# Kernel tuning notes

Hardware: AMD Instinct MI355X
Metric: run time of the kernel (lower is better)

Reference implementation:

```python
import jax, jax.numpy as jnp
import numpy as np

ALIGN_CORNERS = True
APPLY_SMOOTHSTEP = True

SIZES = [(32, 32, 32), (64, 64, 64), (128, 128, 128), (256, 256, 256)]
FEAT_DIMS = [4, 4, 4, 4]
N_POINTS = 1048576  # 2**20 sample points (e.g. 8192 rays x 128 samples)


def setup_inputs() -> dict:
    key = jax.random.key(0)
    ks = jax.random.split(key, 1 + len(SIZES))
    # grid_sample-style coords in [-1, 1], layout [1, 1, 1, N, 3] (x, y, z)
    grid = jax.random.uniform(ks[0], (1, 1, 1, N_POINTS, 3), dtype=jnp.float32) * 2.0 - 1.0
    inp = {"grid": grid}
    for i, (size, c) in enumerate(zip(SIZES, FEAT_DIMS)):
        # original init: (rand(1,C,1,1,1)*2-1).repeat over spatial; use randn volumes for a
        # non-degenerate baseline (same shapes/math path)
        inp[f"vol{i}"] = jax.random.normal(ks[1 + i], (1, c, *size), dtype=jnp.float32)
    return inp


def _smooth_sample(vol, grid_pts):
    """Trilinear sample with border padding, align_corners=True, smoothstep weights.

    vol: [C, D, H, W]; grid_pts: [P, 3] with (x, y, z) in [-1, 1].
    Returns [C, P].
    """
    C, D, H, W = vol.shape
    # unnormalize (align_corners=True): [-1,1] -> [0, dim-1]; border padding via clip
    x = jnp.clip((grid_pts[:, 0] + 1.0) * 0.5 * (W - 1), 0.0, W - 1)
    y = jnp.clip((grid_pts[:, 1] + 1.0) * 0.5 * (H - 1), 0.0, H - 1)
    z = jnp.clip((grid_pts[:, 2] + 1.0) * 0.5 * (D - 1), 0.0, D - 1)

    x0 = jnp.floor(x); y0 = jnp.floor(y); z0 = jnp.floor(z)
    tx = x - x0; ty = y - y0; tz = z - z0
    if APPLY_SMOOTHSTEP:
        tx = tx * tx * (3.0 - 2.0 * tx)
        ty = ty * ty * (3.0 - 2.0 * ty)
        tz = tz * tz * (3.0 - 2.0 * tz)

    x0i = x0.astype(jnp.int32); x1i = jnp.minimum(x0i + 1, W - 1)
    y0i = y0.astype(jnp.int32); y1i = jnp.minimum(y0i + 1, H - 1)
    z0i = z0.astype(jnp.int32); z1i = jnp.minimum(z0i + 1, D - 1)

    # 8 corner gathers -> [C, P]
    c000 = vol[:, z0i, y0i, x0i]; c001 = vol[:, z0i, y0i, x1i]
    c010 = vol[:, z0i, y1i, x0i]; c011 = vol[:, z0i, y1i, x1i]
    c100 = vol[:, z1i, y0i, x0i]; c101 = vol[:, z1i, y0i, x1i]
    c110 = vol[:, z1i, y1i, x0i]; c111 = vol[:, z1i, y1i, x1i]

    c00 = c000 + (c001 - c000) * tx
    c01 = c010 + (c011 - c010) * tx
    c10 = c100 + (c101 - c100) * tx
    c11 = c110 + (c111 - c110) * tx
    c0 = c00 + (c01 - c00) * ty
    c1 = c10 + (c11 - c10) * ty
    return c0 + (c1 - c0) * tz


def reference(grid, vol0, vol1, vol2, vol3):
    # grid: [1, 1, 1, N, 3] -> [N, 3]
    pts = grid.reshape(-1, 3)
    n = pts.shape[0]
    out = []
    for vol in (vol0, vol1, vol2, vol3):
        feat = _smooth_sample(vol[0], pts)            # [C, N]
        out.append(feat.reshape(1, -1, 1, 1, n))      # grid_sample output layout
    return jnp.concatenate(out, axis=1)               # [1, sum(C), 1, 1, N]
```

## Files before the change

### kernel.cpp

```cpp
#include <hip/hip_runtime.h>

#define NPTS 1048576
#define NB 32
#define NBINS (NB * NB * NB)

typedef float v4f __attribute__((ext_vector_type(4)));

__device__ __forceinline__ void nt_store4(const float4& f, float4* p) {
    __builtin_nontemporal_store(*(const v4f*)&f, (v4f*)p);
}


__device__ __forceinline__ float4 lerp4(const float4 a, const float4 b, const float t) {
    return make_float4(a.x + (b.x - a.x) * t,
                       a.y + (b.y - a.y) * t,
                       a.z + (b.z - a.z) * t,
                       a.w + (b.w - a.w) * t);
}

struct CoordW { float tx, ty, tz; int b00, b01, b10, b11, x0, x1; };

template<int D>
__device__ __forceinline__ CoordW mkcoord(float gx, float gy, float gz) {
    CoordW c;
    float x = fminf(fmaxf((gx + 1.0f) * (0.5f * (float)(D - 1)), 0.0f), (float)(D - 1));
    float y = fminf(fmaxf((gy + 1.0f) * (0.5f * (float)(D - 1)), 0.0f), (float)(D - 1));
    float z = fminf(fmaxf((gz + 1.0f) * (0.5f * (float)(D - 1)), 0.0f), (float)(D - 1));
    float xf = floorf(x), yf = floorf(y), zf = floorf(z);
    float tx = x - xf, ty = y - yf, tz = z - zf;
    c.tx = tx * tx * (3.0f - 2.0f * tx);
    c.ty = ty * ty * (3.0f - 2.0f * ty);
    c.tz = tz * tz * (3.0f - 2.0f * tz);
    int x0 = (int)xf, y0 = (int)yf, z0 = (int)zf;
    int y1 = min(y0 + 1, D - 1), z1 = min(z0 + 1, D - 1);
    c.x0 = x0;
    c.x1 = min(x0 + 1, D - 1);
    c.b00 = (z0 * D + y0) * D;
    c.b01 = (z0 * D + y1) * D;
    c.b10 = (z1 * D + y0) * D;
    c.b11 = (z1 * D + y1) * D;
    return c;
}

__device__ __forceinline__ float4 reduce8(const float4* q, const CoordW& c) {
    float4 c00 = lerp4(q[0], q[1], c.tx);
    float4 c01 = lerp4(q[2], q[3], c.tx);
    float4 c10 = lerp4(q[4], q[5], c.tx);
    float4 c11 = lerp4(q[6], q[7], c.tx);
    float4 c0 = lerp4(c00, c01, c.ty);
    float4 c1 = lerp4(c10, c11, c.ty);
    return lerp4(c0, c1, c.tz);
}


#define DHW0 (32 * 32 * 32)
#define DHW1 (64 * 64 * 64)
#define DHW2 (128 * 128 * 128)

__global__ __launch_bounds__(256) void xpose_all_kernel(
    const float* __restrict__ v0, const float* __restrict__ v1, const float* __restrict__ v2,
    float4* __restrict__ w0, float4* __restrict__ w1, float4* __restrict__ w2)
{
    constexpr int B2 = DHW2 / 256, B1 = DHW1 / 256;
    int b = blockIdx.x;
    int t = threadIdx.x;
    if (b < B2) {
        int v = b * 256 + t;
        w2[v] = make_float4(v2[v], v2[v + DHW2], v2[v + 2 * DHW2], v2[v + 3 * DHW2]);
    } else if (b < B2 + B1) {
        int v = (b - B2) * 256 + t;
        w1[v] = make_float4(v1[v], v1[v + DHW1], v1[v + 2 * DHW1], v1[v + 3 * DHW1]);
    } else {
        int v = (b - B2 - B1) * 256 + t;
        w0[v] = make_float4(v0[v], v0[v + DHW0], v0[v + 2 * DHW0], v0[v + 3 * DHW0]);
    }
}


__device__ __forceinline__ int bin_of(float gx, float gy, float gz) {
    float ux = fminf(fmaxf((gx + 1.0f) * 0.5f, 0.0f), 1.0f);
    float uy = fminf(fmaxf((gy + 1.0f) * 0.5f, 0.0f), 1.0f);
    float uz = fminf(fmaxf((gz + 1.0f) * 0.5f, 0.0f), 1.0f);
    int bx = min((int)(ux * (float)NB), NB - 1);
    int by = min((int)(uy * (float)NB), NB - 1);
    int bz = min((int)(uz * (float)NB), NB - 1);
    return (bz * NB + by) * NB + bx;
}

__global__ __launch_bounds__(256) void bin_hist_kernel(const float* __restrict__ grid,
                                                       unsigned* __restrict__ hist) {
    int p = blockIdx.x * blockDim.x + threadIdx.x;
    float gx = grid[3 * p + 0];
    float gy = grid[3 * p + 1];
    float gz = grid[3 * p + 2];
    atomicAdd(&hist[bin_of(gx, gy, gz)], 1u);
}

__global__ __launch_bounds__(1024) void scan_kernel(const unsigned* __restrict__ hist,
                                                    unsigned* __restrict__ offsets) {
    __shared__ unsigned partial[1024];
    const int t = threadIdx.x;
    const int base = t * 32;
    unsigned sum = 0;
#pragma unroll
    for (int i = 0; i < 32; ++i) sum += hist[base + i];
    partial[t] = sum;
    __syncthreads();
    for (int off = 1; off < 1024; off <<= 1) {
        unsigned v = (t >= off) ? partial[t - off] : 0u;
        __syncthreads();
        partial[t] += v;
        __syncthreads();
    }
    unsigned run = partial[t] - sum;
#pragma unroll
    for (int i = 0; i < 32; ++i) {
        offsets[base + i] = run;
        run += hist[base + i];
    }
}

__global__ __launch_bounds__(256) void scatter_kernel(const float* __restrict__ grid,
                                                      unsigned* __restrict__ offsets,
                                                      float4* __restrict__ sorted,
                                                      int* __restrict__ inv) {
    int p = blockIdx.x * blockDim.x + threadIdx.x;
    float gx = grid[3 * p + 0];
    float gy = grid[3 * p + 1];
    float gz = grid[3 * p + 2];
    int b = bin_of(gx, gy, gz);
    unsigned pos = atomicAdd(&offsets[b], 1u);
    sorted[pos] = make_float4(gx, gy, gz, __int_as_float(p));
    inv[p] = (int)pos;
}


__global__ __launch_bounds__(256, 4) void gather_sorted_kernel(
    const float4* __restrict__ sorted,
    const float4* __restrict__ w0, const float4* __restrict__ w1,
    const float4* __restrict__ w2, const float* __restrict__ v3,
    float4* __restrict__ wsout)
{
    int bid = blockIdx.x;
    int sb = (bid & 7) * (int)(gridDim.x >> 3) + (bid >> 3);
    int s = sb * 256 + (int)threadIdx.x;
    float4 gp = sorted[s];
    float gx = gp.x, gy = gp.y, gz = gp.z;

    CoordW c0 = mkcoord<32>(gx, gy, gz);
    CoordW c1 = mkcoord<64>(gx, gy, gz);
    CoordW c2 = mkcoord<128>(gx, gy, gz);
    CoordW c3 = mkcoord<256>(gx, gy, gz);

    float4 qa[8], qb[8], qc[8];
    qa[0] = w0[c0.b00 + c0.x0]; qa[1] = w0[c0.b00 + c0.x1];
    qa[2] = w0[c0.b01 + c0.x0]; qa[3] = w0[c0.b01 + c0.x1];
    qa[4] = w0[c0.b10 + c0.x0]; qa[5] = w0[c0.b10 + c0.x1];
    qa[6] = w0[c0.b11 + c0.x0]; qa[7] = w0[c0.b11 + c0.x1];

    qb[0] = w1[c1.b00 + c1.x0]; qb[1] = w1[c1.b00 + c1.x1];
    qb[2] = w1[c1.b01 + c1.x0]; qb[3] = w1[c1.b01 + c1.x1];
    qb[4] = w1[c1.b10 + c1.x0]; qb[5] = w1[c1.b10 + c1.x1];
    qb[6] = w1[c1.b11 + c1.x0]; qb[7] = w1[c1.b11 + c1.x1];

    qc[0] = w2[c2.b00 + c2.x0]; qc[1] = w2[c2.b00 + c2.x1];
    qc[2] = w2[c2.b01 + c2.x0]; qc[3] = w2[c2.b01 + c2.x1];
    qc[4] = w2[c2.b10 + c2.x0]; qc[5] = w2[c2.b10 + c2.x1];
    qc[6] = w2[c2.b11 + c2.x0]; qc[7] = w2[c2.b11 + c2.x1];

    const int xm = min(c3.x0, 254);
    const bool edge = (c3.x0 == 255);
    float2 qd[16];
#pragma unroll
    for (int ch = 0; ch < 4; ++ch) {
        const float* __restrict__ vc = v3 + (size_t)ch * (256 * 256 * 256);
        qd[ch * 4 + 0] = *(const float2*)(vc + c3.b00 + xm);
        qd[ch * 4 + 1] = *(const float2*)(vc + c3.b01 + xm);
        qd[ch * 4 + 2] = *(const float2*)(vc + c3.b10 + xm);
        qd[ch * 4 + 3] = *(const float2*)(vc + c3.b11 + xm);
    }

    float4 f0 = reduce8(qa, c0);
    float4 f1 = reduce8(qb, c1);
    float4 f2 = reduce8(qc, c2);

    float r3[4];
#pragma unroll
    for (int ch = 0; ch < 4; ++ch) {
        float v00a = edge ? qd[ch * 4 + 0].y : qd[ch * 4 + 0].x, v00b = qd[ch * 4 + 0].y;
        float v01a = edge ? qd[ch * 4 + 1].y : qd[ch * 4 + 1].x, v01b = qd[ch * 4 + 1].y;
        float v10a = edge ? qd[ch * 4 + 2].y : qd[ch * 4 + 2].x, v10b = qd[ch * 4 + 2].y;
        float v11a = edge ? qd[ch * 4 + 3].y : qd[ch * 4 + 3].x, v11b = qd[ch * 4 + 3].y;
        float c00 = v00a + (v00b - v00a) * c3.tx;
        float c01 = v01a + (v01b - v01a) * c3.tx;
        float c10 = v10a + (v10b - v10a) * c3.tx;
        float c11 = v11a + (v11b - v11a) * c3.tx;
        float e0 = c00 + (c01 - c00) * c3.ty;
        float e1 = c10 + (c11 - c10) * c3.ty;
        r3[ch] = e0 + (e1 - e0) * c3.tz;
    }
    float4 f3 = make_float4(r3[0], r3[1], r3[2], r3[3]);

    float4* w = wsout + (size_t)s * 4;
    nt_store4(f0, w + 0);
    nt_store4(f1, w + 1);
    nt_store4(f2, w + 2);
    nt_store4(f3, w + 3);
}


__device__ __forceinline__ void permute_one(const float4* __restrict__ wsout,
                                            const int* __restrict__ inv,
                                            float* __restrict__ out, int p) {
    int s = inv[p];
    const float4* w = wsout + (size_t)s * 4;
    float4 f0 = w[0], f1 = w[1], f2 = w[2], f3 = w[3];
    __builtin_nontemporal_store(f0.x, &out[ 0 * NPTS + p]);
    __builtin_nontemporal_store(f0.y, &out[ 1 * NPTS + p]);
    __builtin_nontemporal_store(f0.z, &out[ 2 * NPTS + p]);
    __builtin_nontemporal_store(f0.w, &out[ 3 * NPTS + p]);
    __builtin_nontemporal_store(f1.x, &out[ 4 * NPTS + p]);
    __builtin_nontemporal_store(f1.y, &out[ 5 * NPTS + p]);
    __builtin_nontemporal_store(f1.z, &out[ 6 * NPTS + p]);
    __builtin_nontemporal_store(f1.w, &out[ 7 * NPTS + p]);
    __builtin_nontemporal_store(f2.x, &out[ 8 * NPTS + p]);
    __builtin_nontemporal_store(f2.y, &out[ 9 * NPTS + p]);
    __builtin_nontemporal_store(f2.z, &out[10 * NPTS + p]);
    __builtin_nontemporal_store(f2.w, &out[11 * NPTS + p]);
    __builtin_nontemporal_store(f3.x, &out[12 * NPTS + p]);
    __builtin_nontemporal_store(f3.y, &out[13 * NPTS + p]);
    __builtin_nontemporal_store(f3.z, &out[14 * NPTS + p]);
    __builtin_nontemporal_store(f3.w, &out[15 * NPTS + p]);
}

__global__ __launch_bounds__(256) void permute_kernel(const float4* __restrict__ wsout,
                                                      const int* __restrict__ inv,
                                                      float* __restrict__ out) {
    int p = blockIdx.x * blockDim.x + threadIdx.x;
    permute_one(wsout, inv, out, p);
    permute_one(wsout, inv, out, p + NPTS / 2);
}


template<int D>
__device__ __forceinline__ float4 sample_inter(const float4* __restrict__ v,
                                               float gx, float gy, float gz) {
    CoordW c = mkcoord<D>(gx, gy, gz);
    float4 q[8];
    q[0] = v[c.b00 + c.x0]; q[1] = v[c.b00 + c.x1];
    q[2] = v[c.b01 + c.x0]; q[3] = v[c.b01 + c.x1];
    q[4] = v[c.b10 + c.x0]; q[5] = v[c.b10 + c.x1];
    q[6] = v[c.b11 + c.x0]; q[7] = v[c.b11 + c.x1];
    return reduce8(q, c);
}

template<int D>
__device__ __forceinline__ float4 sample_direct(const float* __restrict__ v,
                                                float gx, float gy, float gz) {
    CoordW c = mkcoord<D>(gx, gy, gz);
    float r[4];
#pragma unroll
    for (int ch = 0; ch < 4; ++ch) {
        const float* __restrict__ vc = v + (size_t)ch * (D * D * D);
        float c000 = vc[c.b00 + c.x0], c001 = vc[c.b00 + c.x1];
        float c010 = vc[c.b01 + c.x0], c011 = vc[c.b01 + c.x1];
        float c100 = vc[c.b10 + c.x0], c101 = vc[c.b10 + c.x1];
        float c110 = vc[c.b11 + c.x0], c111 = vc[c.b11 + c.x1];
        float c00 = c000 + (c001 - c000) * c.tx;
        float c01 = c010 + (c011 - c010) * c.tx;
        float c10 = c100 + (c101 - c100) * c.tx;
        float c11 = c110 + (c111 - c110) * c.tx;
        float e0 = c00 + (c01 - c00) * c.ty;
        float e1 = c10 + (c11 - c10) * c.ty;
        r[ch] = e0 + (e1 - e0) * c.tz;
    }
    return make_float4(r[0], r[1], r[2], r[3]);
}

__global__ __launch_bounds__(256) void mg_direct_kernel(
    const float* __restrict__ grid,
    const float* __restrict__ v0, const float* __restrict__ v1,
    const float* __restrict__ v2, const float* __restrict__ v3,
    float* __restrict__ out)
{
    int p = blockIdx.x * blockDim.x + threadIdx.x;
    float gx = grid[3 * p + 0];
    float gy = grid[3 * p + 1];
    float gz = grid[3 * p + 2];
    float4 f0 = sample_direct<32>(v0, gx, gy, gz);
    float4 f1 = sample_direct<64>(v1, gx, gy, gz);
    float4 f2 = sample_direct<128>(v2, gx, gy, gz);
    float4 f3 = sample_direct<256>(v3, gx, gy, gz);
    out[ 0 * NPTS + p] = f0.x; out[ 1 * NPTS + p] = f0.y;
    out[ 2 * NPTS + p] = f0.z; out[ 3 * NPTS + p] = f0.w;
    out[ 4 * NPTS + p] = f1.x; out[ 5 * NPTS + p] = f1.y;
    out[ 6 * NPTS + p] = f1.z; out[ 7 * NPTS + p] = f1.w;
    out[ 8 * NPTS + p] = f2.x; out[ 9 * NPTS + p] = f2.y;
    out[10 * NPTS + p] = f2.z; out[11 * NPTS + p] = f2.w;
    out[12 * NPTS + p] = f3.x; out[13 * NPTS + p] = f3.y;
    out[14 * NPTS + p] = f3.z; out[15 * NPTS + p] = f3.w;
}

__global__ __launch_bounds__(256) void mg_inter_kernel(
    const float* __restrict__ grid,
    const float4* __restrict__ w0, const float4* __restrict__ w1,
    const float4* __restrict__ w2, const float* __restrict__ v3,
    float* __restrict__ out)
{
    int p = blockIdx.x * blockDim.x + threadIdx.x;
    float gx = grid[3 * p + 0];
    float gy = grid[3 * p + 1];
    float gz = grid[3 * p + 2];
    float4 f0 = sample_inter<32>(w0, gx, gy, gz);
    float4 f1 = sample_inter<64>(w1, gx, gy, gz);
    float4 f2 = sample_inter<128>(w2, gx, gy, gz);
    float4 f3 = sample_direct<256>(v3, gx, gy, gz);
    out[ 0 * NPTS + p] = f0.x; out[ 1 * NPTS + p] = f0.y;
    out[ 2 * NPTS + p] = f0.z; out[ 3 * NPTS + p] = f0.w;
    out[ 4 * NPTS + p] = f1.x; out[ 5 * NPTS + p] = f1.y;
    out[ 6 * NPTS + p] = f1.z; out[ 7 * NPTS + p] = f1.w;
    out[ 8 * NPTS + p] = f2.x; out[ 9 * NPTS + p] = f2.y;
    out[10 * NPTS + p] = f2.z; out[11 * NPTS + p] = f2.w;
    out[12 * NPTS + p] = f3.x; out[13 * NPTS + p] = f3.y;
    out[14 * NPTS + p] = f3.z; out[15 * NPTS + p] = f3.w;
}


extern "C" void kernel_launch(void* const* d_in, const int* in_sizes, int n_in,
                              void* d_out, int out_size, void* d_ws, size_t ws_size,
                              hipStream_t stream) {
    const float* grid = (const float*)d_in[0];
    const float* v0   = (const float*)d_in[1];
    const float* v1   = (const float*)d_in[2];
    const float* v2   = (const float*)d_in[3];
    const float* v3   = (const float*)d_in[4];
    float* out = (float*)d_out;

    constexpr size_t OFF_WSOUT  = 0;
    constexpr size_t OFF_SORTED = OFF_WSOUT  + (size_t)NPTS * 64;
    constexpr size_t OFF_W2     = OFF_SORTED + (size_t)NPTS * 16;
    constexpr size_t OFF_W1     = OFF_W2     + (size_t)DHW2 * 16;
    constexpr size_t OFF_W0     = OFF_W1     + (size_t)DHW1 * 16;
    constexpr size_t OFF_INV    = OFF_W0     + (size_t)DHW0 * 16;
    constexpr size_t OFF_HIST   = OFF_INV    + (size_t)NPTS * 4;
    constexpr size_t OFF_OFFS   = OFF_HIST   + (size_t)NBINS * 4;
    constexpr size_t WS_FULL    = OFF_OFFS   + (size_t)NBINS * 4;
    constexpr size_t WS_INTER   = (size_t)(DHW0 + DHW1 + DHW2) * 16;

    const int threads = 256;
    const int pt_blocks = NPTS / threads;
    char* ws = (char*)d_ws;

    if (ws_size >= WS_FULL) {
        float4*   wsout  = (float4*)(ws + OFF_WSOUT);
        float4*   sorted = (float4*)(ws + OFF_SORTED);
        float4*   w2     = (float4*)(ws + OFF_W2);
        float4*   w1     = (float4*)(ws + OFF_W1);
        float4*   w0     = (float4*)(ws + OFF_W0);
        int*      inv    = (int*)   (ws + OFF_INV);
        unsigned* hist   = (unsigned*)(ws + OFF_HIST);
        unsigned* offs   = (unsigned*)(ws + OFF_OFFS);

        (void)hipMemsetAsync(hist, 0, (size_t)NBINS * 4, stream);
        xpose_all_kernel<<<(DHW0 + DHW1 + DHW2) / threads, threads, 0, stream>>>(
            v0, v1, v2, w0, w1, w2);
        bin_hist_kernel<<<pt_blocks, threads, 0, stream>>>(grid, hist);
        scan_kernel<<<1, 1024, 0, stream>>>(hist, offs);
        scatter_kernel<<<pt_blocks, threads, 0, stream>>>(grid, offs, sorted, inv);
        gather_sorted_kernel<<<pt_blocks, threads, 0, stream>>>(sorted, w0, w1, w2, v3, wsout);
        permute_kernel<<<pt_blocks / 2, threads, 0, stream>>>(wsout, inv, out);
    } else if (ws_size >= WS_INTER) {
        float4* w0 = (float4*)d_ws;
        float4* w1 = w0 + DHW0;
        float4* w2 = w1 + DHW1;
        xpose_all_kernel<<<(DHW0 + DHW1 + DHW2) / threads, threads, 0, stream>>>(
            v0, v1, v2, w0, w1, w2);
        mg_inter_kernel<<<pt_blocks, threads, 0, stream>>>(grid, w0, w1, w2, v3, out);
    } else {
        mg_direct_kernel<<<pt_blocks, threads, 0, stream>>>(grid, v0, v1, v2, v3, out);
    }
}
```

Baseline: 662.8 us.

## Fuse transpose with histogram, process two points per thread in gather and permute

Merges the volume-transpose and bin-histogram kernels into one launch, removing a kernel boundary. The sorted gather kernel now handles two points per thread, issuing all corner loads for both before any reduction (enforced with a sched_barrier) to raise memory-level parallelism, with launch bounds relaxed from 4 to 3 waves. The permute kernel handles four points per thread with all loads issued before the stores, and gather results now use regular stores instead of nontemporal ones. The cost is higher register pressure and fewer resident waves per CU.

```diff
diff --git a/kernel.cpp b/kernel.cpp
--- a/kernel.cpp
+++ b/kernel.cpp
@@ -4,11 +4,11 @@
 #define NB 32
 #define NBINS (NB * NB * NB)
 
+#define DHW0 (32 * 32 * 32)
+#define DHW1 (64 * 64 * 64)
+#define DHW2 (128 * 128 * 128)
+
 typedef float v4f __attribute__((ext_vector_type(4)));
-
-__device__ __forceinline__ void nt_store4(const float4& f, float4* p) {
-    __builtin_nontemporal_store(*(const v4f*)&f, (v4f*)p);
-}
 
 
 __device__ __forceinline__ float4 lerp4(const float4 a, const float4 b, const float t) {
@@ -52,16 +52,43 @@
     return lerp4(c0, c1, c.tz);
 }
 
-
-#define DHW0 (32 * 32 * 32)
-#define DHW1 (64 * 64 * 64)
-#define DHW2 (128 * 128 * 128)
-
-__global__ __launch_bounds__(256) void xpose_all_kernel(
+__device__ __forceinline__ float4 reduce_v3(const float2* qd, const CoordW& c, bool edge) {
+    float r[4];
+#pragma unroll
+    for (int ch = 0; ch < 4; ++ch) {
+        float v00a = edge ? qd[ch * 4 + 0].y : qd[ch * 4 + 0].x, v00b = qd[ch * 4 + 0].y;
+        float v01a = edge ? qd[ch * 4 + 1].y : qd[ch * 4 + 1].x, v01b = qd[ch * 4 + 1].y;
+        float v10a = edge ? qd[ch * 4 + 2].y : qd[ch * 4 + 2].x, v10b = qd[ch * 4 + 2].y;
+        float v11a = edge ? qd[ch * 4 + 3].y : qd[ch * 4 + 3].x, v11b = qd[ch * 4 + 3].y;
+        float c00 = v00a + (v00b - v00a) * c.tx;
+        float c01 = v01a + (v01b - v01a) * c.tx;
+        float c10 = v10a + (v10b - v10a) * c.tx;
+        float c11 = v11a + (v11b - v11a) * c.tx;
+        float e0 = c00 + (c01 - c00) * c.ty;
+        float e1 = c10 + (c11 - c10) * c.ty;
+        r[ch] = e0 + (e1 - e0) * c.tz;
+    }
+    return make_float4(r[0], r[1], r[2], r[3]);
+}
+
+
+__device__ __forceinline__ int bin_of(float gx, float gy, float gz) {
+    float ux = fminf(fmaxf((gx + 1.0f) * 0.5f, 0.0f), 1.0f);
+    float uy = fminf(fmaxf((gy + 1.0f) * 0.5f, 0.0f), 1.0f);
+    float uz = fminf(fmaxf((gz + 1.0f) * 0.5f, 0.0f), 1.0f);
+    int bx = min((int)(ux * (float)NB), NB - 1);
+    int by = min((int)(uy * (float)NB), NB - 1);
+    int bz = min((int)(uz * (float)NB), NB - 1);
+    return (bz * NB + by) * NB + bx;
+}
+
+
+__global__ __launch_bounds__(256) void xpose_hist_kernel(
     const float* __restrict__ v0, const float* __restrict__ v1, const float* __restrict__ v2,
-    float4* __restrict__ w0, float4* __restrict__ w1, float4* __restrict__ w2)
+    float4* __restrict__ w0, float4* __restrict__ w1, float4* __restrict__ w2,
+    const float* __restrict__ grid, unsigned* __restrict__ hist)
 {
-    constexpr int B2 = DHW2 / 256, B1 = DHW1 / 256;
+    constexpr int B2 = DHW2 / 256, B1 = DHW1 / 256, B0 = DHW0 / 256;
     int b = blockIdx.x;
     int t = threadIdx.x;
     if (b < B2) {
@@ -70,30 +97,16 @@
     } else if (b < B2 + B1) {
         int v = (b - B2) * 256 + t;
         w1[v] = make_float4(v1[v], v1[v + DHW1], v1[v + 2 * DHW1], v1[v + 3 * DHW1]);
-    } else {
+    } else if (b < B2 + B1 + B0) {
         int v = (b - B2 - B1) * 256 + t;
         w0[v] = make_float4(v0[v], v0[v + DHW0], v0[v + 2 * DHW0], v0[v + 3 * DHW0]);
-    }
-}
-
-
-__device__ __forceinline__ int bin_of(float gx, float gy, float gz) {
-    float ux = fminf(fmaxf((gx + 1.0f) * 0.5f, 0.0f), 1.0f);
-    float uy = fminf(fmaxf((gy + 1.0f) * 0.5f, 0.0f), 1.0f);
-    float uz = fminf(fmaxf((gz + 1.0f) * 0.5f, 0.0f), 1.0f);
-    int bx = min((int)(ux * (float)NB), NB - 1);
-    int by = min((int)(uy * (float)NB), NB - 1);
-    int bz = min((int)(uz * (float)NB), NB - 1);
-    return (bz * NB + by) * NB + bx;
-}
-
-__global__ __launch_bounds__(256) void bin_hist_kernel(const float* __restrict__ grid,
-                                                       unsigned* __restrict__ hist) {
-    int p = blockIdx.x * blockDim.x + threadIdx.x;
-    float gx = grid[3 * p + 0];
-    float gy = grid[3 * p + 1];
-    float gz = grid[3 * p + 2];
-    atomicAdd(&hist[bin_of(gx, gy, gz)], 1u);
+    } else {
+        int p = (b - B2 - B1 - B0) * 256 + t;
+        float gx = grid[3 * p + 0];
+        float gy = grid[3 * p + 1];
+        float gz = grid[3 * p + 2];
+        atomicAdd(&hist[bin_of(gx, gy, gz)], 1u);
+    }
 }
 
 __global__ __launch_bounds__(1024) void scan_kernel(const unsigned* __restrict__ hist,
@@ -135,7 +148,7 @@
 }
 
 
-__global__ __launch_bounds__(256, 4) void gather_sorted_kernel(
+__global__ __launch_bounds__(256, 3) void gather_sorted_kernel(
     const float4* __restrict__ sorted,
     const float4* __restrict__ w0, const float4* __restrict__ w1,
     const float4* __restrict__ w2, const float* __restrict__ v3,
@@ -143,78 +156,96 @@
 {
     int bid = blockIdx.x;
     int sb = (bid & 7) * (int)(gridDim.x >> 3) + (bid >> 3);
-    int s = sb * 256 + (int)threadIdx.x;
-    float4 gp = sorted[s];
-    float gx = gp.x, gy = gp.y, gz = gp.z;
-
-    CoordW c0 = mkcoord<32>(gx, gy, gz);
-    CoordW c1 = mkcoord<64>(gx, gy, gz);
-    CoordW c2 = mkcoord<128>(gx, gy, gz);
-    CoordW c3 = mkcoord<256>(gx, gy, gz);
-
-    float4 qa[8], qb[8], qc[8];
-    qa[0] = w0[c0.b00 + c0.x0]; qa[1] = w0[c0.b00 + c0.x1];
-    qa[2] = w0[c0.b01 + c0.x0]; qa[3] = w0[c0.b01 + c0.x1];
-    qa[4] = w0[c0.b10 + c0.x0]; qa[5] = w0[c0.b10 + c0.x1];
-    qa[6] = w0[c0.b11 + c0.x0]; qa[7] = w0[c0.b11 + c0.x1];
-
-    qb[0] = w1[c1.b00 + c1.x0]; qb[1] = w1[c1.b00 + c1.x1];
-    qb[2] = w1[c1.b01 + c1.x0]; qb[3] = w1[c1.b01 + c1.x1];
-    qb[4] = w1[c1.b10 + c1.x0]; qb[5] = w1[c1.b10 + c1.x1];
-    qb[6] = w1[c1.b11 + c1.x0]; qb[7] = w1[c1.b11 + c1.x1];
-
-    qc[0] = w2[c2.b00 + c2.x0]; qc[1] = w2[c2.b00 + c2.x1];
-    qc[2] = w2[c2.b01 + c2.x0]; qc[3] = w2[c2.b01 + c2.x1];
-    qc[4] = w2[c2.b10 + c2.x0]; qc[5] = w2[c2.b10 + c2.x1];
-    qc[6] = w2[c2.b11 + c2.x0]; qc[7] = w2[c2.b11 + c2.x1];
-
-    const int xm = min(c3.x0, 254);
-    const bool edge = (c3.x0 == 255);
-    float2 qd[16];
+    int base = sb * 512 + (int)threadIdx.x;
+    int sA = base, sB = base + 256;
+    float4 gpA = sorted[sA];
+    float4 gpB = sorted[sB];
+
+    CoordW c0A = mkcoord<32>(gpA.x, gpA.y, gpA.z);
+    CoordW c1A = mkcoord<64>(gpA.x, gpA.y, gpA.z);
+    CoordW c2A = mkcoord<128>(gpA.x, gpA.y, gpA.z);
+    CoordW c3A = mkcoord<256>(gpA.x, gpA.y, gpA.z);
+    CoordW c0B = mkcoord<32>(gpB.x, gpB.y, gpB.z);
+    CoordW c1B = mkcoord<64>(gpB.x, gpB.y, gpB.z);
+    CoordW c2B = mkcoord<128>(gpB.x, gpB.y, gpB.z);
+    CoordW c3B = mkcoord<256>(gpB.x, gpB.y, gpB.z);
+    const int  xmA = min(c3A.x0, 254);
+    const bool edgeA = (c3A.x0 == 255);
+    const int  xmB = min(c3B.x0, 254);
+    const bool edgeB = (c3B.x0 == 255);
+
+    float4 qaA[8], qbA[8], qcA[8];
+    float2 qdA[16];
+    float4 qaB[8], qbB[8], qcB[8];
+    float2 qdB[16];
+
+    qaA[0] = w0[c0A.b00 + c0A.x0]; qaA[1] = w0[c0A.b00 + c0A.x1];
+    qaA[2] = w0[c0A.b01 + c0A.x0]; qaA[3] = w0[c0A.b01 + c0A.x1];
+    qaA[4] = w0[c0A.b10 + c0A.x0]; qaA[5] = w0[c0A.b10 + c0A.x1];
+    qaA[6] = w0[c0A.b11 + c0A.x0]; qaA[7] = w0[c0A.b11 + c0A.x1];
+
+    qbA[0] = w1[c1A.b00 + c1A.x0]; qbA[1] = w1[c1A.b00 + c1A.x1];
+    qbA[2] = w1[c1A.b01 + c1A.x0]; qbA[3] = w1[c1A.b01 + c1A.x1];
+    qbA[4] = w1[c1A.b10 + c1A.x0]; qbA[5] = w1[c1A.b10 + c1A.x1];
+    qbA[6] = w1[c1A.b11 + c1A.x0]; qbA[7] = w1[c1A.b11 + c1A.x1];
+
+    qcA[0] = w2[c2A.b00 + c2A.x0]; qcA[1] = w2[c2A.b00 + c2A.x1];
+    qcA[2] = w2[c2A.b01 + c2A.x0]; qcA[3] = w2[c2A.b01 + c2A.x1];
+    qcA[4] = w2[c2A.b10 + c2A.x0]; qcA[5] = w2[c2A.b10 + c2A.x1];
+    qcA[6] = w2[c2A.b11 + c2A.x0]; qcA[7] = w2[c2A.b11 + c2A.x1];
+
 #pragma unroll
     for (int ch = 0; ch < 4; ++ch) {
         const float* __restrict__ vc = v3 + (size_t)ch * (256 * 256 * 256);
-        qd[ch * 4 + 0] = *(const float2*)(vc + c3.b00 + xm);
-        qd[ch * 4 + 1] = *(const float2*)(vc + c3.b01 + xm);
-        qd[ch * 4 + 2] = *(const float2*)(vc + c3.b10 + xm);
-        qd[ch * 4 + 3] = *(const float2*)(vc + c3.b11 + xm);
-    }
-
-    float4 f0 = reduce8(qa, c0);
-    float4 f1 = reduce8(qb, c1);
-    float4 f2 = reduce8(qc, c2);
-
-    float r3[4];
+        qdA[ch * 4 + 0] = *(const float2*)(vc + c3A.b00 + xmA);
+        qdA[ch * 4 + 1] = *(const float2*)(vc + c3A.b01 + xmA);
+        qdA[ch * 4 + 2] = *(const float2*)(vc + c3A.b10 + xmA);
+        qdA[ch * 4 + 3] = *(const float2*)(vc + c3A.b11 + xmA);
+    }
+
+    qaB[0] = w0[c0B.b00 + c0B.x0]; qaB[1] = w0[c0B.b00 + c0B.x1];
+    qaB[2] = w0[c0B.b01 + c0B.x0]; qaB[3] = w0[c0B.b01 + c0B.x1];
+    qaB[4] = w0[c0B.b10 + c0B.x0]; qaB[5] = w0[c0B.b10 + c0B.x1];
+    qaB[6] = w0[c0B.b11 + c0B.x0]; qaB[7] = w0[c0B.b11 + c0B.x1];
+
+    qbB[0] = w1[c1B.b00 + c1B.x0]; qbB[1] = w1[c1B.b00 + c1B.x1];
+    qbB[2] = w1[c1B.b01 + c1B.x0]; qbB[3] = w1[c1B.b01 + c1B.x1];
+    qbB[4] = w1[c1B.b10 + c1B.x0]; qbB[5] = w1[c1B.b10 + c1B.x1];
+    qbB[6] = w1[c1B.b11 + c1B.x0]; qbB[7] = w1[c1B.b11 + c1B.x1];
+
+    qcB[0] = w2[c2B.b00 + c2B.x0]; qcB[1] = w2[c2B.b00 + c2B.x1];
+    qcB[2] = w2[c2B.b01 + c2B.x0]; qcB[3] = w2[c2B.b01 + c2B.x1];
+    qcB[4] = w2[c2B.b10 + c2B.x0]; qcB[5] = w2[c2B.b10 + c2B.x1];
+    qcB[6] = w2[c2B.b11 + c2B.x0]; qcB[7] = w2[c2B.b11 + c2B.x1];
+
 #pragma unroll
     for (int ch = 0; ch < 4; ++ch) {
-        float v00a = edge ? qd[ch * 4 + 0].y : qd[ch * 4 + 0].x, v00b = qd[ch * 4 + 0].y;
-        float v01a = edge ? qd[ch * 4 + 1].y : qd[ch * 4 + 1].x, v01b = qd[ch * 4 + 1].y;
-        float v10a = edge ? qd[ch * 4 + 2].y : qd[ch * 4 + 2].x, v10b = qd[ch * 4 + 2].y;
-        float v11a = edge ? qd[ch * 4 + 3].y : qd[ch * 4 + 3].x, v11b = qd[ch * 4 + 3].y;
-        float c00 = v00a + (v00b - v00a) * c3.tx;
-        float c01 = v01a + (v01b - v01a) * c3.tx;
-        float c10 = v10a + (v10b - v10a) * c3.tx;
-        float c11 = v11a + (v11b - v11a) * c3.tx;
-        float e0 = c00 + (c01 - c00) * c3.ty;
-        float e1 = c10 + (c11 - c10) * c3.ty;
-        r3[ch] = e0 + (e1 - e0) * c3.tz;
-    }
-    float4 f3 = make_float4(r3[0], r3[1], r3[2], r3[3]);
-
-    float4* w = wsout + (size_t)s * 4;
-    nt_store4(f0, w + 0);
-    nt_store4(f1, w + 1);
-    nt_store4(f2, w + 2);
-    nt_store4(f3, w + 3);
-}
-
-
-__device__ __forceinline__ void permute_one(const float4* __restrict__ wsout,
-                                            const int* __restrict__ inv,
-                                            float* __restrict__ out, int p) {
-    int s = inv[p];
-    const float4* w = wsout + (size_t)s * 4;
-    float4 f0 = w[0], f1 = w[1], f2 = w[2], f3 = w[3];
+        const float* __restrict__ vc = v3 + (size_t)ch * (256 * 256 * 256);
+        qdB[ch * 4 + 0] = *(const float2*)(vc + c3B.b00 + xmB);
+        qdB[ch * 4 + 1] = *(const float2*)(vc + c3B.b01 + xmB);
+        qdB[ch * 4 + 2] = *(const float2*)(vc + c3B.b10 + xmB);
+        qdB[ch * 4 + 3] = *(const float2*)(vc + c3B.b11 + xmB);
+    }
+
+    __builtin_amdgcn_sched_barrier(0);
+
+    float4* wA = wsout + (size_t)sA * 4;
+    wA[0] = reduce8(qaA, c0A);
+    wA[1] = reduce8(qbA, c1A);
+    wA[2] = reduce8(qcA, c2A);
+    wA[3] = reduce_v3(qdA, c3A, edgeA);
+
+    float4* wB = wsout + (size_t)sB * 4;
+    wB[0] = reduce8(qaB, c0B);
+    wB[1] = reduce8(qbB, c1B);
+    wB[2] = reduce8(qcB, c2B);
+    wB[3] = reduce_v3(qdB, c3B, edgeB);
+}
+
+
+__device__ __forceinline__ void store16(const float4 f0, const float4 f1,
+                                        const float4 f2, const float4 f3,
+                                        float* __restrict__ out, int p) {
     __builtin_nontemporal_store(f0.x, &out[ 0 * NPTS + p]);
     __builtin_nontemporal_store(f0.y, &out[ 1 * NPTS + p]);
     __builtin_nontemporal_store(f0.z, &out[ 2 * NPTS + p]);
@@ -237,8 +268,21 @@
                                                       const int* __restrict__ inv,
                                                       float* __restrict__ out) {
     int p = blockIdx.x * blockDim.x + threadIdx.x;
-    permute_one(wsout, inv, out, p);
-    permute_one(wsout, inv, out, p + NPTS / 2);
+    int pA = p, pB = p + NPTS / 4, pC = p + NPTS / 2, pD = p + 3 * (NPTS / 4);
+    int sA = inv[pA], sB = inv[pB], sC = inv[pC], sD = inv[pD];
+    const float4* wA = wsout + (size_t)sA * 4;
+    const float4* wB = wsout + (size_t)sB * 4;
+    const float4* wC = wsout + (size_t)sC * 4;
+    const float4* wD = wsout + (size_t)sD * 4;
+    float4 a0 = wA[0], a1 = wA[1], a2 = wA[2], a3 = wA[3];
+    float4 b0 = wB[0], b1 = wB[1], b2 = wB[2], b3 = wB[3];
+    float4 c0 = wC[0], c1 = wC[1], c2 = wC[2], c3 = wC[3];
+    float4 d0 = wD[0], d1 = wD[1], d2 = wD[2], d3 = wD[3];
+    __builtin_amdgcn_sched_barrier(0);
+    store16(a0, a1, a2, a3, out, pA);
+    store16(b0, b1, b2, b3, out, pB);
+    store16(c0, c1, c2, c3, out, pC);
+    store16(d0, d1, d2, d3, out, pD);
 }
 
 
@@ -362,19 +406,20 @@
         unsigned* offs   = (unsigned*)(ws + OFF_OFFS);
 
         (void)hipMemsetAsync(hist, 0, (size_t)NBINS * 4, stream);
-        xpose_all_kernel<<<(DHW0 + DHW1 + DHW2) / threads, threads, 0, stream>>>(
-            v0, v1, v2, w0, w1, w2);
-        bin_hist_kernel<<<pt_blocks, threads, 0, stream>>>(grid, hist);
+        const int xh_blocks = (DHW0 + DHW1 + DHW2) / threads + pt_blocks;
+        xpose_hist_kernel<<<xh_blocks, threads, 0, stream>>>(
+            v0, v1, v2, w0, w1, w2, grid, hist);
         scan_kernel<<<1, 1024, 0, stream>>>(hist, offs);
         scatter_kernel<<<pt_blocks, threads, 0, stream>>>(grid, offs, sorted, inv);
-        gather_sorted_kernel<<<pt_blocks, threads, 0, stream>>>(sorted, w0, w1, w2, v3, wsout);
-        permute_kernel<<<pt_blocks / 2, threads, 0, stream>>>(wsout, inv, out);
+        gather_sorted_kernel<<<pt_blocks / 2, threads, 0, stream>>>(
+            sorted, w0, w1, w2, v3, wsout);
+        permute_kernel<<<pt_blocks / 4, threads, 0, stream>>>(wsout, inv, out);
     } else if (ws_size >= WS_INTER) {
         float4* w0 = (float4*)d_ws;
         float4* w1 = w0 + DHW0;
         float4* w2 = w1 + DHW1;
-        xpose_all_kernel<<<(DHW0 + DHW1 + DHW2) / threads, threads, 0, stream>>>(
-            v0, v1, v2, w0, w1, w2);
+        xpose_hist_kernel<<<(DHW0 + DHW1 + DHW2) / threads, threads, 0, stream>>>(
+            v0, v1, v2, w0, w1, w2, grid, (unsigned*)nullptr);
         mg_inter_kernel<<<pt_blocks, threads, 0, stream>>>(grid, w0, w1, w2, v3, out);
     } else {
         mg_direct_kernel<<<pt_blocks, threads, 0, stream>>>(grid, v0, v1, v2, v3, out);
```

After: 647.8 us. 1.02x faster.

## Drop spatial sort pipeline; transpose all volumes to channel-last and fuse sampling

Applied to the files above, without the earlier changes.

Removes the histogram, scan, scatter, sorted-gather and permute stages. Instead it transposes all four volumes, including the 256^3 one, into float4 channel-interleaved layout and samples every level in one fused kernel that writes output directly with nontemporal stores. This drops sort and permute traffic and the extra launches. In exchange it adds a 256 MB transpose pass per call and loses the cache locality that sorting gave the large-volume gathers. It also adds a sched_barrier so all loads issue before the arithmetic, and sets launch bounds to 3 blocks per SM.

```diff
diff --git a/kernel.cpp b/kernel.cpp
--- a/kernel.cpp
+++ b/kernel.cpp
@@ -1,12 +1,15 @@
 #include <hip/hip_runtime.h>
 
 #define NPTS 1048576
-#define NB 32
-#define NBINS (NB * NB * NB)
+
+#define DHW0 (32 * 32 * 32)
+#define DHW1 (64 * 64 * 64)
+#define DHW2 (128 * 128 * 128)
+#define DHW3 (256 * 256 * 256)
 
 typedef float v4f __attribute__((ext_vector_type(4)));
 
-__device__ __forceinline__ void nt_store4(const float4& f, float4* p) {
+__device__ __forceinline__ void nt_store4(const float4 f, float4* p) {
     __builtin_nontemporal_store(*(const v4f*)&f, (v4f*)p);
 }
 
@@ -52,169 +55,28 @@
     return lerp4(c0, c1, c.tz);
 }
 
-
-#define DHW0 (32 * 32 * 32)
-#define DHW1 (64 * 64 * 64)
-#define DHW2 (128 * 128 * 128)
-
-__global__ __launch_bounds__(256) void xpose_all_kernel(
-    const float* __restrict__ v0, const float* __restrict__ v1, const float* __restrict__ v2,
-    float4* __restrict__ w0, float4* __restrict__ w1, float4* __restrict__ w2)
-{
-    constexpr int B2 = DHW2 / 256, B1 = DHW1 / 256;
-    int b = blockIdx.x;
-    int t = threadIdx.x;
-    if (b < B2) {
-        int v = b * 256 + t;
-        w2[v] = make_float4(v2[v], v2[v + DHW2], v2[v + 2 * DHW2], v2[v + 3 * DHW2]);
-    } else if (b < B2 + B1) {
-        int v = (b - B2) * 256 + t;
-        w1[v] = make_float4(v1[v], v1[v + DHW1], v1[v + 2 * DHW1], v1[v + 3 * DHW1]);
-    } else {
-        int v = (b - B2 - B1) * 256 + t;
-        w0[v] = make_float4(v0[v], v0[v + DHW0], v0[v + 2 * DHW0], v0[v + 3 * DHW0]);
-    }
-}
-
-
-__device__ __forceinline__ int bin_of(float gx, float gy, float gz) {
-    float ux = fminf(fmaxf((gx + 1.0f) * 0.5f, 0.0f), 1.0f);
-    float uy = fminf(fmaxf((gy + 1.0f) * 0.5f, 0.0f), 1.0f);
-    float uz = fminf(fmaxf((gz + 1.0f) * 0.5f, 0.0f), 1.0f);
-    int bx = min((int)(ux * (float)NB), NB - 1);
-    int by = min((int)(uy * (float)NB), NB - 1);
-    int bz = min((int)(uz * (float)NB), NB - 1);
-    return (bz * NB + by) * NB + bx;
-}
-
-__global__ __launch_bounds__(256) void bin_hist_kernel(const float* __restrict__ grid,
-                                                       unsigned* __restrict__ hist) {
-    int p = blockIdx.x * blockDim.x + threadIdx.x;
-    float gx = grid[3 * p + 0];
-    float gy = grid[3 * p + 1];
-    float gz = grid[3 * p + 2];
-    atomicAdd(&hist[bin_of(gx, gy, gz)], 1u);
-}
-
-__global__ __launch_bounds__(1024) void scan_kernel(const unsigned* __restrict__ hist,
-                                                    unsigned* __restrict__ offsets) {
-    __shared__ unsigned partial[1024];
-    const int t = threadIdx.x;
-    const int base = t * 32;
-    unsigned sum = 0;
-#pragma unroll
-    for (int i = 0; i < 32; ++i) sum += hist[base + i];
-    partial[t] = sum;
-    __syncthreads();
-    for (int off = 1; off < 1024; off <<= 1) {
-        unsigned v = (t >= off) ? partial[t - off] : 0u;
-        __syncthreads();
-        partial[t] += v;
-        __syncthreads();
-    }
-    unsigned run = partial[t] - sum;
-#pragma unroll
-    for (int i = 0; i < 32; ++i) {
-        offsets[base + i] = run;
-        run += hist[base + i];
-    }
-}
-
-__global__ __launch_bounds__(256) void scatter_kernel(const float* __restrict__ grid,
-                                                      unsigned* __restrict__ offsets,
-                                                      float4* __restrict__ sorted,
-                                                      int* __restrict__ inv) {
-    int p = blockIdx.x * blockDim.x + threadIdx.x;
-    float gx = grid[3 * p + 0];
-    float gy = grid[3 * p + 1];
-    float gz = grid[3 * p + 2];
-    int b = bin_of(gx, gy, gz);
-    unsigned pos = atomicAdd(&offsets[b], 1u);
-    sorted[pos] = make_float4(gx, gy, gz, __int_as_float(p));
-    inv[p] = (int)pos;
-}
-
-
-__global__ __launch_bounds__(256, 4) void gather_sorted_kernel(
-    const float4* __restrict__ sorted,
-    const float4* __restrict__ w0, const float4* __restrict__ w1,
-    const float4* __restrict__ w2, const float* __restrict__ v3,
-    float4* __restrict__ wsout)
-{
-    int bid = blockIdx.x;
-    int sb = (bid & 7) * (int)(gridDim.x >> 3) + (bid >> 3);
-    int s = sb * 256 + (int)threadIdx.x;
-    float4 gp = sorted[s];
-    float gx = gp.x, gy = gp.y, gz = gp.z;
-
-    CoordW c0 = mkcoord<32>(gx, gy, gz);
-    CoordW c1 = mkcoord<64>(gx, gy, gz);
-    CoordW c2 = mkcoord<128>(gx, gy, gz);
-    CoordW c3 = mkcoord<256>(gx, gy, gz);
-
-    float4 qa[8], qb[8], qc[8];
-    qa[0] = w0[c0.b00 + c0.x0]; qa[1] = w0[c0.b00 + c0.x1];
-    qa[2] = w0[c0.b01 + c0.x0]; qa[3] = w0[c0.b01 + c0.x1];
-    qa[4] = w0[c0.b10 + c0.x0]; qa[5] = w0[c0.b10 + c0.x1];
-    qa[6] = w0[c0.b11 + c0.x0]; qa[7] = w0[c0.b11 + c0.x1];
-
-    qb[0] = w1[c1.b00 + c1.x0]; qb[1] = w1[c1.b00 + c1.x1];
-    qb[2] = w1[c1.b01 + c1.x0]; qb[3] = w1[c1.b01 + c1.x1];
-    qb[4] = w1[c1.b10 + c1.x0]; qb[5] = w1[c1.b10 + c1.x1];
-    qb[6] = w1[c1.b11 + c1.x0]; qb[7] = w1[c1.b11 + c1.x1];
-
-    qc[0] = w2[c2.b00 + c2.x0]; qc[1] = w2[c2.b00 + c2.x1];
-    qc[2] = w2[c2.b01 + c2.x0]; qc[3] = w2[c2.b01 + c2.x1];
-    qc[4] = w2[c2.b10 + c2.x0]; qc[5] = w2[c2.b10 + c2.x1];
-    qc[6] = w2[c2.b11 + c2.x0]; qc[7] = w2[c2.b11 + c2.x1];
-
-    const int xm = min(c3.x0, 254);
-    const bool edge = (c3.x0 == 255);
-    float2 qd[16];
-#pragma unroll
-    for (int ch = 0; ch < 4; ++ch) {
-        const float* __restrict__ vc = v3 + (size_t)ch * (256 * 256 * 256);
-        qd[ch * 4 + 0] = *(const float2*)(vc + c3.b00 + xm);
-        qd[ch * 4 + 1] = *(const float2*)(vc + c3.b01 + xm);
-        qd[ch * 4 + 2] = *(const float2*)(vc + c3.b10 + xm);
-        qd[ch * 4 + 3] = *(const float2*)(vc + c3.b11 + xm);
-    }
-
-    float4 f0 = reduce8(qa, c0);
-    float4 f1 = reduce8(qb, c1);
-    float4 f2 = reduce8(qc, c2);
-
-    float r3[4];
+__device__ __forceinline__ float4 reduce_v3(const float2* qd, const CoordW& c, bool edge) {
+    float r[4];
 #pragma unroll
     for (int ch = 0; ch < 4; ++ch) {
         float v00a = edge ? qd[ch * 4 + 0].y : qd[ch * 4 + 0].x, v00b = qd[ch * 4 + 0].y;
         float v01a = edge ? qd[ch * 4 + 1].y : qd[ch * 4 + 1].x, v01b = qd[ch * 4 + 1].y;
         float v10a = edge ? qd[ch * 4 + 2].y : qd[ch * 4 + 2].x, v10b = qd[ch * 4 + 2].y;
         float v11a = edge ? qd[ch * 4 + 3].y : qd[ch * 4 + 3].x, v11b = qd[ch * 4 + 3].y;
-        float c00 = v00a + (v00b - v00a) * c3.tx;
-        float c01 = v01a + (v01b - v01a) * c3.tx;
-        float c10 = v10a + (v10b - v10a) * c3.tx;
-        float c11 = v11a + (v11b - v11a) * c3.tx;
-        float e0 = c00 + (c01 - c00) * c3.ty;
-        float e1 = c10 + (c11 - c10) * c3.ty;
-        r3[ch] = e0 + (e1 - e0) * c3.tz;
-    }
-    float4 f3 = make_float4(r3[0], r3[1], r3[2], r3[3]);
-
-    float4* w = wsout + (size_t)s * 4;
-    nt_store4(f0, w + 0);
-    nt_store4(f1, w + 1);
-    nt_store4(f2, w + 2);
-    nt_store4(f3, w + 3);
-}
-
-
-__device__ __forceinline__ void permute_one(const float4* __restrict__ wsout,
-                                            const int* __restrict__ inv,
-                                            float* __restrict__ out, int p) {
-    int s = inv[p];
-    const float4* w = wsout + (size_t)s * 4;
-    float4 f0 = w[0], f1 = w[1], f2 = w[2], f3 = w[3];
+        float c00 = v00a + (v00b - v00a) * c.tx;
+        float c01 = v01a + (v01b - v01a) * c.tx;
+        float c10 = v10a + (v10b - v10a) * c.tx;
+        float c11 = v11a + (v11b - v11a) * c.tx;
+        float e0 = c00 + (c01 - c00) * c.ty;
+        float e1 = c10 + (c11 - c10) * c.ty;
+        r[ch] = e0 + (e1 - e0) * c.tz;
+    }
+    return make_float4(r[0], r[1], r[2], r[3]);
+}
+
+__device__ __forceinline__ void store16(const float4 f0, const float4 f1,
+                                        const float4 f2, const float4 f3,
+                                        float* __restrict__ out, int p) {
     __builtin_nontemporal_store(f0.x, &out[ 0 * NPTS + p]);
     __builtin_nontemporal_store(f0.y, &out[ 1 * NPTS + p]);
     __builtin_nontemporal_store(f0.z, &out[ 2 * NPTS + p]);
@@ -233,26 +95,150 @@
     __builtin_nontemporal_store(f3.w, &out[15 * NPTS + p]);
 }
 
-__global__ __launch_bounds__(256) void permute_kernel(const float4* __restrict__ wsout,
-                                                      const int* __restrict__ inv,
-                                                      float* __restrict__ out) {
-    int p = blockIdx.x * blockDim.x + threadIdx.x;
-    permute_one(wsout, inv, out, p);
-    permute_one(wsout, inv, out, p + NPTS / 2);
-}
-
-
-template<int D>
-__device__ __forceinline__ float4 sample_inter(const float4* __restrict__ v,
-                                               float gx, float gy, float gz) {
-    CoordW c = mkcoord<D>(gx, gy, gz);
-    float4 q[8];
-    q[0] = v[c.b00 + c.x0]; q[1] = v[c.b00 + c.x1];
-    q[2] = v[c.b01 + c.x0]; q[3] = v[c.b01 + c.x1];
-    q[4] = v[c.b10 + c.x0]; q[5] = v[c.b10 + c.x1];
-    q[6] = v[c.b11 + c.x0]; q[7] = v[c.b11 + c.x1];
-    return reduce8(q, c);
-}
+
+__global__ __launch_bounds__(256) void xpose_kernel(
+    const float* __restrict__ v0, const float* __restrict__ v1,
+    const float* __restrict__ v2, const float* __restrict__ v3,
+    float4* __restrict__ w0, float4* __restrict__ w1,
+    float4* __restrict__ w2, float4* __restrict__ w3)
+{
+    constexpr int B2 = DHW2 / 256, B1 = DHW1 / 256, B0 = DHW0 / 256;
+    int b = blockIdx.x;
+    int t = threadIdx.x;
+    if (b < B2) {
+        int v = b * 256 + t;
+        w2[v] = make_float4(v2[v], v2[v + DHW2], v2[v + 2 * DHW2], v2[v + 3 * DHW2]);
+    } else if (b < B2 + B1) {
+        int v = (b - B2) * 256 + t;
+        w1[v] = make_float4(v1[v], v1[v + DHW1], v1[v + 2 * DHW1], v1[v + 3 * DHW1]);
+    } else if (b < B2 + B1 + B0) {
+        int v = (b - B2 - B1) * 256 + t;
+        w0[v] = make_float4(v0[v], v0[v + DHW0], v0[v + 2 * DHW0], v0[v + 3 * DHW0]);
+    } else {
+        int v = (b - B2 - B1 - B0) * 256 + t;
+        nt_store4(make_float4(v3[v], v3[v + DHW3], v3[v + 2 * DHW3], v3[v + 3 * DHW3]),
+                  w3 + v);
+    }
+}
+
+
+__global__ __launch_bounds__(256, 3) void mg_fused_kernel(
+    const float* __restrict__ grid,
+    const float4* __restrict__ w0, const float4* __restrict__ w1,
+    const float4* __restrict__ w2, const float* __restrict__ v3,
+    float* __restrict__ out)
+{
+    int p = blockIdx.x * 256 + (int)threadIdx.x;
+    float gx = grid[3 * p + 0];
+    float gy = grid[3 * p + 1];
+    float gz = grid[3 * p + 2];
+
+    CoordW c0 = mkcoord<32>(gx, gy, gz);
+    CoordW c1 = mkcoord<64>(gx, gy, gz);
+    CoordW c2 = mkcoord<128>(gx, gy, gz);
+    CoordW c3 = mkcoord<256>(gx, gy, gz);
+    const int  xm = min(c3.x0, 254);
+    const bool edge = (c3.x0 == 255);
+
+    float4 qa[8], qb[8], qc[8];
+    float2 qd[16];
+
+    qa[0] = w0[c0.b00 + c0.x0]; qa[1] = w0[c0.b00 + c0.x1];
+    qa[2] = w0[c0.b01 + c0.x0]; qa[3] = w0[c0.b01 + c0.x1];
+    qa[4] = w0[c0.b10 + c0.x0]; qa[5] = w0[c0.b10 + c0.x1];
+    qa[6] = w0[c0.b11 + c0.x0]; qa[7] = w0[c0.b11 + c0.x1];
+
+    qb[0] = w1[c1.b00 + c1.x0]; qb[1] = w1[c1.b00 + c1.x1];
+    qb[2] = w1[c1.b01 + c1.x0]; qb[3] = w1[c1.b01 + c1.x1];
+    qb[4] = w1[c1.b10 + c1.x0]; qb[5] = w1[c1.b10 + c1.x1];
+    qb[6] = w1[c1.b11 + c1.x0]; qb[7] = w1[c1.b11 + c1.x1];
+
+    qc[0] = w2[c2.b00 + c2.x0]; qc[1] = w2[c2.b00 + c2.x1];
+    qc[2] = w2[c2.b01 + c2.x0]; qc[3] = w2[c2.b01 + c2.x1];
+    qc[4] = w2[c2.b10 + c2.x0]; qc[5] = w2[c2.b10 + c2.x1];
+    qc[6] = w2[c2.b11 + c2.x0]; qc[7] = w2[c2.b11 + c2.x1];
+
+#pragma unroll
+    for (int ch = 0; ch < 4; ++ch) {
+        const float* __restrict__ vc = v3 + (size_t)ch * DHW3;
+        qd[ch * 4 + 0] = *(const float2*)(vc + c3.b00 + xm);
+        qd[ch * 4 + 1] = *(const float2*)(vc + c3.b01 + xm);
+        qd[ch * 4 + 2] = *(const float2*)(vc + c3.b10 + xm);
+        qd[ch * 4 + 3] = *(const float2*)(vc + c3.b11 + xm);
+    }
+
+    __builtin_amdgcn_sched_barrier(0);
+
+    float4 f0 = reduce8(qa, c0);
+    float4 f1 = reduce8(qb, c1);
+    float4 f2 = reduce8(qc, c2);
+    float4 f3 = reduce_v3(qd, c3, edge);
+
+    store16(f0, f1, f2, f3, out, p);
+}
+
+
+__global__ __launch_bounds__(256, 3) void mg_fused_w3_kernel(
+    const float* __restrict__ grid,
+    const float4* __restrict__ w0, const float4* __restrict__ w1,
+    const float4* __restrict__ w2, const float4* __restrict__ w3,
+    float* __restrict__ out)
+{
+    int p = blockIdx.x * 256 + (int)threadIdx.x;
+    float gx = grid[3 * p + 0];
+    float gy = grid[3 * p + 1];
+    float gz = grid[3 * p + 2];
+
+    CoordW c0 = mkcoord<32>(gx, gy, gz);
+    CoordW c1 = mkcoord<64>(gx, gy, gz);
+    CoordW c2 = mkcoord<128>(gx, gy, gz);
+    CoordW c3 = mkcoord<256>(gx, gy, gz);
+    const int  xm = min(c3.x0, 254);
+    const bool edge = (c3.x0 == 255);
+
+    float4 qa[8], qb[8], qc[8], qlo[4], qhi[4];
+
+    qa[0] = w0[c0.b00 + c0.x0]; qa[1] = w0[c0.b00 + c0.x1];
+    qa[2] = w0[c0.b01 + c0.x0]; qa[3] = w0[c0.b01 + c0.x1];
+    qa[4] = w0[c0.b10 + c0.x0]; qa[5] = w0[c0.b10 + c0.x1];
+    qa[6] = w0[c0.b11 + c0.x0]; qa[7] = w0[c0.b11 + c0.x1];
+
+    qb[0] = w1[c1.b00 + c1.x0]; qb[1] = w1[c1.b00 + c1.x1];
+    qb[2] = w1[c1.b01 + c1.x0]; qb[3] = w1[c1.b01 + c1.x1];
+    qb[4] = w1[c1.b10 + c1.x0]; qb[5] = w1[c1.b10 + c1.x1];
+    qb[6] = w1[c1.b11 + c1.x0]; qb[7] = w1[c1.b11 + c1.x1];
+
+    qc[0] = w2[c2.b00 + c2.x0]; qc[1] = w2[c2.b00 + c2.x1];
+    qc[2] = w2[c2.b01 + c2.x0]; qc[3] = w2[c2.b01 + c2.x1];
+    qc[4] = w2[c2.b10 + c2.x0]; qc[5] = w2[c2.b10 + c2.x1];
+    qc[6] = w2[c2.b11 + c2.x0]; qc[7] = w2[c2.b11 + c2.x1];
+
+    qlo[0] = w3[c3.b00 + xm]; qhi[0] = w3[c3.b00 + xm + 1];
+    qlo[1] = w3[c3.b01 + xm]; qhi[1] = w3[c3.b01 + xm + 1];
+    qlo[2] = w3[c3.b10 + xm]; qhi[2] = w3[c3.b10 + xm + 1];
+    qlo[3] = w3[c3.b11 + xm]; qhi[3] = w3[c3.b11 + xm + 1];
+
+    __builtin_amdgcn_sched_barrier(0);
+
+    float4 f0 = reduce8(qa, c0);
+    float4 f1 = reduce8(qb, c1);
+    float4 f2 = reduce8(qc, c2);
+
+    float4 a00 = edge ? qhi[0] : qlo[0];
+    float4 a01 = edge ? qhi[1] : qlo[1];
+    float4 a10 = edge ? qhi[2] : qlo[2];
+    float4 a11 = edge ? qhi[3] : qlo[3];
+    float4 r00 = lerp4(a00, qhi[0], c3.tx);
+    float4 r01 = lerp4(a01, qhi[1], c3.tx);
+    float4 r10 = lerp4(a10, qhi[2], c3.tx);
+    float4 r11 = lerp4(a11, qhi[3], c3.tx);
+    float4 e0 = lerp4(r00, r01, c3.ty);
+    float4 e1 = lerp4(r10, r11, c3.ty);
+    float4 f3 = lerp4(e0, e1, c3.tz);
+
+    store16(f0, f1, f2, f3, out, p);
+}
+
 
 template<int D>
 __device__ __forceinline__ float4 sample_direct(const float* __restrict__ v,
@@ -291,38 +277,7 @@
     float4 f1 = sample_direct<64>(v1, gx, gy, gz);
     float4 f2 = sample_direct<128>(v2, gx, gy, gz);
     float4 f3 = sample_direct<256>(v3, gx, gy, gz);
-    out[ 0 * NPTS + p] = f0.x; out[ 1 * NPTS + p] = f0.y;
-    out[ 2 * NPTS + p] = f0.z; out[ 3 * NPTS + p] = f0.w;
-    out[ 4 * NPTS + p] = f1.x; out[ 5 * NPTS + p] = f1.y;
-    out[ 6 * NPTS + p] = f1.z; out[ 7 * NPTS + p] = f1.w;
-    out[ 8 * NPTS + p] = f2.x; out[ 9 * NPTS + p] = f2.y;
-    out[10 * NPTS + p] = f2.z; out[11 * NPTS + p] = f2.w;
-    out[12 * NPTS + p] = f3.x; out[13 * NPTS + p] = f3.y;
-    out[14 * NPTS + p] = f3.z; out[15 * NPTS + p] = f3.w;
-}
-
-__global__ __launch_bounds__(256) void mg_inter_kernel(
-    const float* __restrict__ grid,
-    const float4* __restrict__ w0, const float4* __restrict__ w1,
-    const float4* __restrict__ w2, const float* __restrict__ v3,
-    float* __restrict__ out)
-{
-    int p = blockIdx.x * blockDim.x + threadIdx.x;
-    float gx = grid[3 * p + 0];
-    float gy = grid[3 * p + 1];
-    float gz = grid[3 * p + 2];
-    float4 f0 = sample_inter<32>(w0, gx, gy, gz);
-    float4 f1 = sample_inter<64>(w1, gx, gy, gz);
-    float4 f2 = sample_inter<128>(w2, gx, gy, gz);
-    float4 f3 = sample_direct<256>(v3, gx, gy, gz);
-    out[ 0 * NPTS + p] = f0.x; out[ 1 * NPTS + p] = f0.y;
-    out[ 2 * NPTS + p] = f0.z; out[ 3 * NPTS + p] = f0.w;
-    out[ 4 * NPTS + p] = f1.x; out[ 5 * NPTS + p] = f1.y;
-    out[ 6 * NPTS + p] = f1.z; out[ 7 * NPTS + p] = f1.w;
-    out[ 8 * NPTS + p] = f2.x; out[ 9 * NPTS + p] = f2.y;
-    out[10 * NPTS + p] = f2.z; out[11 * NPTS + p] = f2.w;
-    out[12 * NPTS + p] = f3.x; out[13 * NPTS + p] = f3.y;
-    out[14 * NPTS + p] = f3.z; out[15 * NPTS + p] = f3.w;
+    store16(f0, f1, f2, f3, out, p);
 }
 
 
@@ -336,46 +291,31 @@
     const float* v3   = (const float*)d_in[4];
     float* out = (float*)d_out;
 
-    constexpr size_t OFF_WSOUT  = 0;
-    constexpr size_t OFF_SORTED = OFF_WSOUT  + (size_t)NPTS * 64;
-    constexpr size_t OFF_W2     = OFF_SORTED + (size_t)NPTS * 16;
-    constexpr size_t OFF_W1     = OFF_W2     + (size_t)DHW2 * 16;
-    constexpr size_t OFF_W0     = OFF_W1     + (size_t)DHW1 * 16;
-    constexpr size_t OFF_INV    = OFF_W0     + (size_t)DHW0 * 16;
-    constexpr size_t OFF_HIST   = OFF_INV    + (size_t)NPTS * 4;
-    constexpr size_t OFF_OFFS   = OFF_HIST   + (size_t)NBINS * 4;
-    constexpr size_t WS_FULL    = OFF_OFFS   + (size_t)NBINS * 4;
-    constexpr size_t WS_INTER   = (size_t)(DHW0 + DHW1 + DHW2) * 16;
+    constexpr size_t WS_INTER = (size_t)(DHW0 + DHW1 + DHW2) * 16;
+    constexpr size_t WS_W3    = WS_INTER + (size_t)DHW3 * 16;
 
     const int threads = 256;
     const int pt_blocks = NPTS / threads;
-    char* ws = (char*)d_ws;
-
-    if (ws_size >= WS_FULL) {
-        float4*   wsout  = (float4*)(ws + OFF_WSOUT);
-        float4*   sorted = (float4*)(ws + OFF_SORTED);
-        float4*   w2     = (float4*)(ws + OFF_W2);
-        float4*   w1     = (float4*)(ws + OFF_W1);
-        float4*   w0     = (float4*)(ws + OFF_W0);
-        int*      inv    = (int*)   (ws + OFF_INV);
-        unsigned* hist   = (unsigned*)(ws + OFF_HIST);
-        unsigned* offs   = (unsigned*)(ws + OFF_OFFS);
-
-        (void)hipMemsetAsync(hist, 0, (size_t)NBINS * 4, stream);
-        xpose_all_kernel<<<(DHW0 + DHW1 + DHW2) / threads, threads, 0, stream>>>(
-            v0, v1, v2, w0, w1, w2);
-        bin_hist_kernel<<<pt_blocks, threads, 0, stream>>>(grid, hist);
-        scan_kernel<<<1, 1024, 0, stream>>>(hist, offs);
-        scatter_kernel<<<pt_blocks, threads, 0, stream>>>(grid, offs, sorted, inv);
-        gather_sorted_kernel<<<pt_blocks, threads, 0, stream>>>(sorted, w0, w1, w2, v3, wsout);
-        permute_kernel<<<pt_blocks / 2, threads, 0, stream>>>(wsout, inv, out);
+    constexpr int xb_small = (DHW0 + DHW1 + DHW2) / 256;
+    constexpr int xb_v3    = DHW3 / 256;
+
+    if (ws_size >= WS_W3) {
+        float4* w0 = (float4*)d_ws;
+        float4* w1 = w0 + DHW0;
+        float4* w2 = w1 + DHW1;
+        float4* w3 = w2 + DHW2;
+        xpose_kernel<<<xb_small + xb_v3, threads, 0, stream>>>(
+            v0, v1, v2, v3, w0, w1, w2, w3);
+        mg_fused_w3_kernel<<<pt_blocks, threads, 0, stream>>>(
+            grid, w0, w1, w2, w3, out);
     } else if (ws_size >= WS_INTER) {
         float4* w0 = (float4*)d_ws;
         float4* w1 = w0 + DHW0;
         float4* w2 = w1 + DHW1;
-        xpose_all_kernel<<<(DHW0 + DHW1 + DHW2) / threads, threads, 0, stream>>>(
-            v0, v1, v2, w0, w1, w2);
-        mg_inter_kernel<<<pt_blocks, threads, 0, stream>>>(grid, w0, w1, w2, v3, out);
+        xpose_kernel<<<xb_small, threads, 0, stream>>>(
+            v0, v1, v2, v3, w0, w1, w2, (float4*)nullptr);
+        mg_fused_kernel<<<pt_blocks, threads, 0, stream>>>(
+            grid, w0, w1, w2, v3, out);
     } else {
         mg_direct_kernel<<<pt_blocks, threads, 0, stream>>>(grid, v0, v1, v2, v3, out);
     }
```

Measured after the change: 680.1 us. 1.03x slower.
